# Performance work log

Measured on AMD Instinct MI355X. Metric: run time of the kernel, lower is better.

Reference implementation:

```python
import jax, jax.numpy as jnp
import numpy as np

B, N_IN, N_MID, N_OUT = 262144, 64, 128, 32


def setup_inputs() -> dict:
    key = jax.random.key(0)
    kx, k1, kb1, k2, kb2 = jax.random.split(key, 5)
    v1 = 1.0 / np.sqrt(N_IN)   # per-synapse init range sqrt(1/len(dendrites))
    v2 = 1.0 / np.sqrt(N_MID)
    return {
        "x": jax.random.normal(kx, (B, N_IN), dtype=jnp.float32),
        "W1": jax.random.uniform(k1, (N_IN, N_MID), minval=-v1, maxval=v1, dtype=jnp.float32),
        "b1": jnp.zeros((N_MID,), dtype=jnp.float32),  # obtain_float_parameter inits biases to 0.0
        "W2": jax.random.uniform(k2, (N_MID, N_OUT), minval=-v2, maxval=v2, dtype=jnp.float32),
        "b2": jnp.zeros((N_OUT,), dtype=jnp.float32),
    }


def reference(x, W1, b1, W2, b2):
    # RegularNeuron: sum_i k_ij * x_i + b_j, then ReLU
    h = jax.nn.relu(x @ W1 + b1)          # [B, N_MID]
    # Output DestinationNeuron: sum_j k_jo * h_j + b_o, no activation
    y = h @ W2 + b2                        # [B, N_OUT]
    return y
```

## Files before the change

kernel.cpp:

```cpp
#include <hip/hip_runtime.h>
#include <hip/hip_bf16.h>

#define B_ROWS 262144
#define N_TILES (B_ROWS / 16)

typedef short short8 __attribute__((ext_vector_type(8)));
typedef float f32x4 __attribute__((ext_vector_type(4)));

__device__ inline short f2bf(float f) {
    __hip_bfloat16 h = __float2bfloat16(f);
    return __builtin_bit_cast(short, h);
}
__device__ inline unsigned pk2(float a, float b) {
    unsigned lo = (unsigned short)f2bf(a);
    unsigned hi = (unsigned short)f2bf(b);
    return lo | (hi << 16);
}

__global__ __launch_bounds__(256, 2) void livenet_mlp(
    const float* __restrict__ x, const float* __restrict__ W1,
    const float* __restrict__ b1, const float* __restrict__ W2,
    const float* __restrict__ b2, float* __restrict__ y) {
    __shared__ __align__(16) short hbuf[4 * 2048];
    __shared__ __align__(16) short w1t[128 * 64];
    __shared__ __align__(16) short w2t[32 * 128];
    __shared__ __align__(16) float bls[160];

    const int tid  = threadIdx.x;
    const int wid  = tid >> 6;
    const int lane = tid & 63;
    const int g    = lane >> 4;
    const int q    = lane & 15;
    short* hb = hbuf + wid * 2048;
    const int key = 2 * (q & 7);

#pragma unroll
    for (int p = 0; p < 8; ++p) {
        const int idx = p * 1024 + tid * 4;
        f32x4 v = *(const f32x4*)(W1 + idx);
        const int k = idx >> 7, c = idx & 127;
#pragma unroll
        for (int e = 0; e < 4; ++e) w1t[(c + e) * 64 + k] = f2bf(v[e]);
    }
#pragma unroll
    for (int p = 0; p < 4; ++p) {
        const int idx = p * 1024 + tid * 4;
        f32x4 v = *(const f32x4*)(W2 + idx);
        const int k = idx >> 5, o = idx & 31;
#pragma unroll
        for (int e = 0; e < 4; ++e) w2t[(o + e) * 128 + k] = f2bf(v[e]);
    }
    if (tid < 128) bls[tid] = b1[tid];
    else if (tid < 160) bls[tid] = b2[tid - 128];
    __syncthreads();

    short8 w1f[2][8];
#pragma unroll
    for (int ks = 0; ks < 2; ++ks)
#pragma unroll
        for (int n = 0; n < 8; ++n)
            w1f[ks][n] = *(const short8*)&w1t[(n * 16 + q) * 64 + ks * 32 + g * 8];
    short8 w2f[4][2];
#pragma unroll
    for (int ks = 0; ks < 4; ++ks)
#pragma unroll
        for (int n = 0; n < 2; ++n)
            w2f[ks][n] = *(const short8*)&w2t[(n * 16 + q) * 128 + ks * 32 + g * 8];
    f32x4 binit1[8], binit2[2];
#pragma unroll
    for (int n = 0; n < 8; ++n) binit1[n] = *(const f32x4*)&bls[n * 16 + 4 * g];
#pragma unroll
    for (int n = 0; n < 2; ++n) binit2[n] = *(const f32x4*)&bls[128 + n * 16 + 4 * g];

    const int gwave = blockIdx.x * 4 + wid;
    const int S     = gridDim.x * 4;
    const float* xl = x + (size_t)q * 64 + g * 8;

    f32x4 c0, c1, c2, c3;
    {
        const f32x4* p = (const f32x4*)(xl + (size_t)gwave * 1024);
        c0 = p[0]; c1 = p[1]; c2 = p[8]; c3 = p[9];
    }

    for (int tile = gwave; tile < N_TILES; tile += S) {
        const int tn = (tile + S < N_TILES) ? (tile + S) : tile;
        f32x4 p0, p1, p2, p3;
        {
            const f32x4* pp = (const f32x4*)(xl + (size_t)tn * 1024);
            p0 = pp[0]; p1 = pp[1]; p2 = pp[8]; p3 = pp[9];
        }

        const int row0 = tile * 16;

        short8 a0, a1;
        {
            short8 v;
            v[0] = f2bf(c0[0]); v[1] = f2bf(c0[1]); v[2] = f2bf(c0[2]); v[3] = f2bf(c0[3]);
            v[4] = f2bf(c1[0]); v[5] = f2bf(c1[1]); v[6] = f2bf(c1[2]); v[7] = f2bf(c1[3]);
            a0 = v;
            v[0] = f2bf(c2[0]); v[1] = f2bf(c2[1]); v[2] = f2bf(c2[2]); v[3] = f2bf(c2[3]);
            v[4] = f2bf(c3[0]); v[5] = f2bf(c3[1]); v[6] = f2bf(c3[2]); v[7] = f2bf(c3[3]);
            a1 = v;
        }

        f32x4 acc1[8];
#pragma unroll
        for (int n = 0; n < 8; ++n) {
            acc1[n] = __builtin_amdgcn_mfma_f32_16x16x32_bf16(w1f[0][n], a0, binit1[n], 0, 0, 0);
            acc1[n] = __builtin_amdgcn_mfma_f32_16x16x32_bf16(w1f[1][n], a1, acc1[n], 0, 0, 0);
        }

#pragma unroll
        for (int n = 0; n < 8; ++n) {
            float h0 = fmaxf(acc1[n][0], 0.0f);
            float h1 = fmaxf(acc1[n][1], 0.0f);
            float h2 = fmaxf(acc1[n][2], 0.0f);
            float h3 = fmaxf(acc1[n][3], 0.0f);
            uint2 w;
            w.x = pk2(h0, h1);
            w.y = pk2(h2, h3);
            const int cbp = (4 * n + g) ^ key;
            ((uint2*)hb)[q * 32 + cbp] = w;
        }

        short8 ha[4];
#pragma unroll
        for (int ks = 0; ks < 4; ++ks) {
            const int cbr = (8 * ks + 2 * g) ^ key;
            ha[ks] = *(const short8*)&hb[q * 128 + 4 * cbr];
        }

        f32x4 acc2[2];
#pragma unroll
        for (int n = 0; n < 2; ++n) {
            acc2[n] = __builtin_amdgcn_mfma_f32_16x16x32_bf16(w2f[0][n], ha[0], binit2[n], 0, 0, 0);
#pragma unroll
            for (int ks = 1; ks < 4; ++ks)
                acc2[n] = __builtin_amdgcn_mfma_f32_16x16x32_bf16(w2f[ks][n], ha[ks], acc2[n], 0, 0, 0);
        }

#pragma unroll
        for (int n = 0; n < 2; ++n)
            *(f32x4*)(y + (size_t)(row0 + q) * 32 + n * 16 + 4 * g) = acc2[n];

        c0 = p0; c1 = p1; c2 = p2; c3 = p3;
    }
}

extern "C" void kernel_launch(void* const* d_in, const int* in_sizes, int n_in,
                              void* d_out, int out_size, void* d_ws, size_t ws_size,
                              hipStream_t stream) {
    const float* x  = (const float*)d_in[0];
    const float* W1 = (const float*)d_in[1];
    const float* b1 = (const float*)d_in[2];
    const float* W2 = (const float*)d_in[3];
    const float* b2 = (const float*)d_in[4];
    float* y = (float*)d_out;

    const int blocks = 512;
    livenet_mlp<<<blocks, 256, 0, stream>>>(x, W1, b1, W2, b2, y);
}
```

Baseline: 28.46 us.

## Fully unroll tile loop with 3-deep register prefetch and nontemporal output stores

Replaces the grid-stride loop with a fixed 8-tile fully unrolled sequence per wave (2048 waves × 8 tiles), prefetching x three tiles ahead in rotating register sets instead of one. Bias initial values are reloaded from LDS per tile rather than held in registers, output stores become nontemporal, and the hidden buffer is accessed as uint2. The aim is more memory-level parallelism on the streaming x reads and less register pressure from bias arrays, at the cost of hardcoding grid size and batch size and raising register use for the extra prefetch buffers.

```diff
diff --git a/kernel.cpp b/kernel.cpp
--- a/kernel.cpp
+++ b/kernel.cpp
@@ -1,11 +1,14 @@
 #include <hip/hip_runtime.h>
 #include <hip/hip_bf16.h>
 
-#define B_ROWS 262144
-#define N_TILES (B_ROWS / 16)
+#define B_ROWS   262144
+#define N_TILES  (B_ROWS / 16)
+#define S_WAVES  2048
+#define TPW      8
 
 typedef short short8 __attribute__((ext_vector_type(8)));
 typedef float f32x4 __attribute__((ext_vector_type(4)));
+struct U2x2 { uint2 a, b; };
 
 __device__ inline short f2bf(float f) {
     __hip_bfloat16 h = __float2bfloat16(f);
@@ -21,7 +24,7 @@
     const float* __restrict__ x, const float* __restrict__ W1,
     const float* __restrict__ b1, const float* __restrict__ W2,
     const float* __restrict__ b2, float* __restrict__ y) {
-    __shared__ __align__(16) short hbuf[4 * 2048];
+    __shared__ __align__(16) uint2 hbu[4 * 512];
     __shared__ __align__(16) short w1t[128 * 64];
     __shared__ __align__(16) short w2t[32 * 128];
     __shared__ __align__(16) float bls[160];
@@ -31,7 +34,7 @@
     const int lane = tid & 63;
     const int g    = lane >> 4;
     const int q    = lane & 15;
-    short* hb = hbuf + wid * 2048;
+    uint2* hb = hbu + wid * 512;
     const int key = 2 * (q & 7);
 
 #pragma unroll
@@ -66,85 +69,95 @@
 #pragma unroll
         for (int n = 0; n < 2; ++n)
             w2f[ks][n] = *(const short8*)&w2t[(n * 16 + q) * 128 + ks * 32 + g * 8];
-    f32x4 binit1[8], binit2[2];
-#pragma unroll
-    for (int n = 0; n < 8; ++n) binit1[n] = *(const f32x4*)&bls[n * 16 + 4 * g];
-#pragma unroll
-    for (int n = 0; n < 2; ++n) binit2[n] = *(const f32x4*)&bls[128 + n * 16 + 4 * g];
 
     const int gwave = blockIdx.x * 4 + wid;
-    const int S     = gridDim.x * 4;
-    const float* xl = x + (size_t)q * 64 + g * 8;
+    const float* xw = x + (size_t)gwave * 1024 + (size_t)q * 64 + g * 8;
+    float*       yw = y + (size_t)(gwave * 16 + q) * 32 + 4 * g;
 
-    f32x4 c0, c1, c2, c3;
-    {
-        const f32x4* p = (const f32x4*)(xl + (size_t)gwave * 1024);
-        c0 = p[0]; c1 = p[1]; c2 = p[8]; c3 = p[9];
+    f32x4 S00, S01, S02, S03, S10, S11, S12, S13, S20, S21, S22, S23;
+
+#define XLOAD(A0, A1, A2, A3, K)                                              \
+    {                                                                         \
+        const f32x4* p_ = (const f32x4*)(xw + (size_t)(K) * 2097152);         \
+        A0 = p_[0]; A1 = p_[1]; A2 = p_[8]; A3 = p_[9];                       \
     }
 
-    for (int tile = gwave; tile < N_TILES; tile += S) {
-        const int tn = (tile + S < N_TILES) ? (tile + S) : tile;
-        f32x4 p0, p1, p2, p3;
-        {
-            const f32x4* pp = (const f32x4*)(xl + (size_t)tn * 1024);
-            p0 = pp[0]; p1 = pp[1]; p2 = pp[8]; p3 = pp[9];
-        }
+    XLOAD(S00, S01, S02, S03, 0)
+    XLOAD(S10, S11, S12, S13, 1)
+    XLOAD(S20, S21, S22, S23, 2)
 
-        const int row0 = tile * 16;
+#define BODY(K, A0, A1, A2, A3)                                               \
+    {                                                                         \
+               \
+        short8 a0, a1;                                                        \
+        {                                                                     \
+            short8 v;                                                         \
+            v[0] = f2bf(A0[0]); v[1] = f2bf(A0[1]);                           \
+            v[2] = f2bf(A0[2]); v[3] = f2bf(A0[3]);                           \
+            v[4] = f2bf(A1[0]); v[5] = f2bf(A1[1]);                           \
+            v[6] = f2bf(A1[2]); v[7] = f2bf(A1[3]);                           \
+            a0 = v;                                                           \
+            v[0] = f2bf(A2[0]); v[1] = f2bf(A2[1]);                           \
+            v[2] = f2bf(A2[2]); v[3] = f2bf(A2[3]);                           \
+            v[4] = f2bf(A3[0]); v[5] = f2bf(A3[1]);                           \
+            v[6] = f2bf(A3[2]); v[7] = f2bf(A3[3]);                           \
+            a1 = v;                                                           \
+        }                                                                     \
+             \
+        if ((K) + 3 < TPW) XLOAD(A0, A1, A2, A3, (K) + 3)                     \
+                        \
+        f32x4 acc1[8];                                                        \
+        _Pragma("unroll")                                                     \
+        for (int n = 0; n < 8; ++n) {                                         \
+            acc1[n] = *(const f32x4*)&bls[n * 16 + 4 * g];                    \
+            acc1[n] = __builtin_amdgcn_mfma_f32_16x16x32_bf16(                \
+                w1f[0][n], a0, acc1[n], 0, 0, 0);                             \
+            acc1[n] = __builtin_amdgcn_mfma_f32_16x16x32_bf16(                \
+                w1f[1][n], a1, acc1[n], 0, 0, 0);                             \
+        }                                                                     \
+             \
+        _Pragma("unroll")                                                     \
+        for (int n = 0; n < 8; ++n) {                                         \
+            uint2 w;                                                          \
+            w.x = pk2(fmaxf(acc1[n][0], 0.0f), fmaxf(acc1[n][1], 0.0f));      \
+            w.y = pk2(fmaxf(acc1[n][2], 0.0f), fmaxf(acc1[n][3], 0.0f));      \
+            hb[q * 32 + ((4 * n + g) ^ key)] = w;                             \
+        }                                                                     \
+              \
+        short8 ha[4];                                                         \
+        _Pragma("unroll")                                                     \
+        for (int ks = 0; ks < 4; ++ks) {                                      \
+            const int jj = q * 32 + ((8 * ks + 2 * g) ^ key);                 \
+            U2x2 t_{hb[jj], hb[jj + 1]};                                      \
+            ha[ks] = __builtin_bit_cast(short8, t_);                          \
+        }                                                                     \
+                        \
+        f32x4 acc2[2];                                                        \
+        _Pragma("unroll")                                                     \
+        for (int n = 0; n < 2; ++n) {                                         \
+            acc2[n] = *(const f32x4*)&bls[128 + n * 16 + 4 * g];              \
+            _Pragma("unroll")                                                 \
+            for (int ks = 0; ks < 4; ++ks)                                    \
+                acc2[n] = __builtin_amdgcn_mfma_f32_16x16x32_bf16(            \
+                    w2f[ks][n], ha[ks], acc2[n], 0, 0, 0);                    \
+        }                                                                     \
+        _Pragma("unroll")                                                     \
+        for (int n = 0; n < 2; ++n)                                           \
+            __builtin_nontemporal_store(                                      \
+                acc2[n], (f32x4*)(yw + (size_t)(K) * 1048576 + n * 16));      \
+    }
 
-        short8 a0, a1;
-        {
-            short8 v;
-            v[0] = f2bf(c0[0]); v[1] = f2bf(c0[1]); v[2] = f2bf(c0[2]); v[3] = f2bf(c0[3]);
-            v[4] = f2bf(c1[0]); v[5] = f2bf(c1[1]); v[6] = f2bf(c1[2]); v[7] = f2bf(c1[3]);
-            a0 = v;
-            v[0] = f2bf(c2[0]); v[1] = f2bf(c2[1]); v[2] = f2bf(c2[2]); v[3] = f2bf(c2[3]);
-            v[4] = f2bf(c3[0]); v[5] = f2bf(c3[1]); v[6] = f2bf(c3[2]); v[7] = f2bf(c3[3]);
-            a1 = v;
-        }
+    BODY(0, S00, S01, S02, S03)
+    BODY(1, S10, S11, S12, S13)
+    BODY(2, S20, S21, S22, S23)
+    BODY(3, S00, S01, S02, S03)
+    BODY(4, S10, S11, S12, S13)
+    BODY(5, S20, S21, S22, S23)
+    BODY(6, S00, S01, S02, S03)
+    BODY(7, S10, S11, S12, S13)
 
-        f32x4 acc1[8];
-#pragma unroll
-        for (int n = 0; n < 8; ++n) {
-            acc1[n] = __builtin_amdgcn_mfma_f32_16x16x32_bf16(w1f[0][n], a0, binit1[n], 0, 0, 0);
-            acc1[n] = __builtin_amdgcn_mfma_f32_16x16x32_bf16(w1f[1][n], a1, acc1[n], 0, 0, 0);
-        }
-
-#pragma unroll
-        for (int n = 0; n < 8; ++n) {
-            float h0 = fmaxf(acc1[n][0], 0.0f);
-            float h1 = fmaxf(acc1[n][1], 0.0f);
-            float h2 = fmaxf(acc1[n][2], 0.0f);
-            float h3 = fmaxf(acc1[n][3], 0.0f);
-            uint2 w;
-            w.x = pk2(h0, h1);
-            w.y = pk2(h2, h3);
-            const int cbp = (4 * n + g) ^ key;
-            ((uint2*)hb)[q * 32 + cbp] = w;
-        }
-
-        short8 ha[4];
-#pragma unroll
-        for (int ks = 0; ks < 4; ++ks) {
-            const int cbr = (8 * ks + 2 * g) ^ key;
-            ha[ks] = *(const short8*)&hb[q * 128 + 4 * cbr];
-        }
-
-        f32x4 acc2[2];
-#pragma unroll
-        for (int n = 0; n < 2; ++n) {
-            acc2[n] = __builtin_amdgcn_mfma_f32_16x16x32_bf16(w2f[0][n], ha[0], binit2[n], 0, 0, 0);
-#pragma unroll
-            for (int ks = 1; ks < 4; ++ks)
-                acc2[n] = __builtin_amdgcn_mfma_f32_16x16x32_bf16(w2f[ks][n], ha[ks], acc2[n], 0, 0, 0);
-        }
-
-#pragma unroll
-        for (int n = 0; n < 2; ++n)
-            *(f32x4*)(y + (size_t)(row0 + q) * 32 + n * 16 + 4 * g) = acc2[n];
-
-        c0 = p0; c1 = p1; c2 = p2; c3 = p3;
-    }
+#undef BODY
+#undef XLOAD
 }
 
 extern "C" void kernel_launch(void* const* d_in, const int* in_sizes, int n_in,
@@ -157,6 +170,5 @@
     const float* b2 = (const float*)d_in[4];
     float* y = (float*)d_out;
 
-    const int blocks = 512;
-    livenet_mlp<<<blocks, 256, 0, stream>>>(x, W1, b1, W2, b2, y);
+    livenet_mlp<<<512, 256, 0, stream>>>(x, W1, b1, W2, b2, y);
 }
```

Result: slower. 31.17 us (+9.5%).
